# Kernel optimization log

Hardware: AMD Instinct MI355X
Metric: run time of the kernel (lower is better)

The kernel has to match this reference:

```python
import jax, jax.numpy as jnp
import numpy as np

N = 12288          # atoms
G = 12             # graphs in batch
R = 1536           # residues
K = 32             # max_num_neighbors
RADIUS = 5.0
MIN_DISTANCE = 5
EPS = 1e-10


def setup_inputs() -> dict:
    key = jax.random.key(0)
    k1, k2, k3 = jax.random.split(key, 3)
    # positions in a 50 A box -> protein-like density (~a few neighbors in r=5)
    node_position = jax.random.uniform(k1, (N, 3), dtype=jnp.float32) * 50.0
    node2graph = jnp.sort(jax.random.randint(k2, (N,), 0, G, dtype=jnp.int32))
    atom2residue = jnp.sort(jax.random.randint(k3, (N,), 0, R, dtype=jnp.int32))
    return {"node_position": node_position, "node2graph": node2graph,
            "atom2residue": atom2residue}


def _select_neighbors(node_position, node2graph):
    """For each node i, pick up to K nearest same-graph nodes within RADIUS.
    Returns idx [N,K] (neighbor indices) and in_radius [N,K] (validity)."""
    n = node_position.shape[0]
    sq = jnp.sum(node_position * node_position, axis=-1)            # [N]
    d2 = sq[:, None] + sq[None, :] - 2.0 * (node_position @ node_position.T)
    d2 = jnp.maximum(d2, 0.0)                                        # [N,N]
    ar = jnp.arange(n)
    valid = (node2graph[:, None] == node2graph[None, :]) \
            & (ar[:, None] != ar[None, :]) \
            & (d2 <= RADIUS * RADIUS)
    nd2 = jnp.where(valid, d2, jnp.inf)
    neg_d2, idx = jax.lax.top_k(-nd2, K)                             # nearest K
    in_radius = jnp.isfinite(neg_d2)
    return idx, in_radius


def reference(node_position, node2graph, atom2residue):
    n = node_position.shape[0]
    idx, in_radius = _select_neighbors(node_position, node2graph)
    node_out = jnp.repeat(jnp.arange(n, dtype=jnp.int32), K)         # center i
    node_in = idx.reshape(-1).astype(jnp.int32)                      # neighbor j
    valid = in_radius.reshape(-1)
    # residue-distance filter: drop |res_in - res_out| < min_distance
    res_diff = jnp.abs(atom2residue[node_in] - atom2residue[node_out])
    valid = valid & (res_diff >= MIN_DISTANCE)
    # drop near-coincident positions (||p_i - p_j|| < eps)
    diff = node_position[node_in] - node_position[node_out]
    d2_sel = jnp.sum(diff * diff, axis=-1)
    valid = valid & (d2_sel >= EPS * EPS)
    relation = jnp.zeros_like(node_in)
    edge_list = jnp.stack([node_in, node_out, relation], axis=-1)    # [N*K,3]
    edge_list = jnp.where(valid[:, None], edge_list, -1)             # pad invalid
    return edge_list, valid, jnp.int32(1)
```

## Files before the change

kernel.cpp:

```cpp
#include <hip/hip_runtime.h>

#define EDGE_K 32
#define CAP    128
#define NB     64

__global__ __launch_bounds__(256) void pack_kernel(
    const float* __restrict__ pos, const int* __restrict__ n2g,
    float4* __restrict__ pk, int* __restrict__ bounds, int n)
{
    int i = blockIdx.x * blockDim.x + threadIdx.x;
    if (i >= n) return;
    pk[i] = make_float4(pos[3*i+0], pos[3*i+1], pos[3*i+2], 0.0f);
    const int gi = n2g[i];
    if (i == 0) {
        for (int g = 0; g <= gi && g < NB; ++g) bounds[g] = 0;
    } else {
        const int gp = n2g[i-1];
        if (gp != gi) for (int g = gp + 1; g <= gi && g < NB; ++g) bounds[g] = i;
    }
    if (i == n - 1) {
        for (int g = gi + 1; g < NB; ++g) bounds[g] = n;
    }
}

__global__ __launch_bounds__(64) void spatial_edge_fast(
    const float4* __restrict__ pk,
    const int* __restrict__ n2g,
    const int* __restrict__ a2r,
    const int* __restrict__ bounds,
    int* __restrict__ out, int n)
{
    const int i    = blockIdx.x;
    const int lane = threadIdx.x;

    __shared__ int2 scand[CAP];
    __shared__ int2 sres[EDGE_K];

    const float4 pi = pk[i];
    const float xi = pi.x, yi = pi.y, zi = pi.z;
    const float si = xi*xi + yi*yi + zi*zi;
    const int g  = n2g[i];
    const int ri = a2r[i];

    int jstart, jend;
    if (g < NB - 1) {
        jstart = bounds[g];
        jend   = bounds[g + 1];
    } else {
        int lo = 0, hi = n;
        while (lo < hi) { int m = (lo + hi) >> 1; if (n2g[m] < g) lo = m + 1; else hi = m; }
        jstart = lo; hi = n;
        while (lo < hi) { int m = (lo + hi) >> 1; if (n2g[m] <= g) lo = m + 1; else hi = m; }
        jend = lo;
    }

    int count = 0;
    auto process = [&](float4 p, int j) {
        bool pass = false; float d2 = 0.0f;
        if (j < jend && j != i) {
            const float sj2 = p.x*p.x + p.y*p.y + p.z*p.z;
            const float dt  = xi*p.x + yi*p.y + zi*p.z;
            d2 = si + sj2 - 2.0f*dt;
            d2 = fmaxf(d2, 0.0f);
            pass = (d2 <= 25.0f);
        }
        const unsigned long long mask = __ballot(pass);
        if (pass) {
            const int idx = count +
                (int)__builtin_amdgcn_mbcnt_hi((unsigned)(mask >> 32),
                     __builtin_amdgcn_mbcnt_lo((unsigned)mask, 0u));
            if (idx < CAP) scand[idx] = make_int2(__float_as_int(d2), j);
        }
        count += __popcll(mask);
    };

    const int nch = (jend - jstart + 63) >> 6;
    const int jm  = jend - 1;
    for (int c = 0; c < nch; c += 4) {
        const int ja = jstart + (c << 6) + lane;
        const float4 p0 = pk[min(ja,       jm)];
        const float4 p1 = pk[min(ja +  64, jm)];
        const float4 p2 = pk[min(ja + 128, jm)];
        const float4 p3 = pk[min(ja + 192, jm)];
        process(p0, ja);
        if (c + 1 < nch) process(p1, ja + 64);
        if (c + 2 < nch) process(p2, ja + 128);
        if (c + 3 < nch) process(p3, ja + 192);
    }
    __syncthreads();

    int cnt = 0;
    if (count <= CAP) {
        const int m = count;
        for (int c = lane; c < m; c += 64) {
            const int2 e = scand[c];
            const float dc = __int_as_float(e.x);
            int rank = 0;
            for (int t = 0; t < m; ++t) {
                const int2 et = scand[t];
                const float dtv = __int_as_float(et.x);
                rank += (dtv < dc) || (dtv == dc && et.y < e.y);
            }
            if (rank < EDGE_K) sres[rank] = e;
        }
        cnt = (m < EDGE_K) ? m : EDGE_K;
    } else {
        if (lane == 0) {
            float bd[EDGE_K]; int bj[EDGE_K]; int c2 = 0;
            for (int j = jstart; j < jend; ++j) {
                if (j == i) continue;
                const float4 p = pk[j];
                const float sj2 = p.x*p.x + p.y*p.y + p.z*p.z;
                const float dt  = xi*p.x + yi*p.y + zi*p.z;
                float d2 = si + sj2 - 2.0f*dt;
                d2 = fmaxf(d2, 0.0f);
                if (d2 > 25.0f) continue;
                if (c2 == EDGE_K && d2 >= bd[EDGE_K-1]) continue;
                int p2 = (c2 < EDGE_K) ? c2 : (EDGE_K - 1);
                while (p2 > 0 && bd[p2-1] > d2) { bd[p2] = bd[p2-1]; bj[p2] = bj[p2-1]; --p2; }
                bd[p2] = d2; bj[p2] = j;
                if (c2 < EDGE_K) ++c2;
            }
            for (int k = 0; k < c2; ++k) sres[k] = make_int2(__float_as_int(bd[k]), bj[k]);
        }
        cnt = (count < EDGE_K) ? count : EDGE_K;
    }
    __syncthreads();

    const int NK = n * EDGE_K;
    int* valid_out = out + 3 * NK;
    if (lane < EDGE_K) {
        const int k = lane;
        int a = -1, b = -1, c = -1, v = 0;
        if (k < cnt) {
            const int j = sres[k].y;
            const int rj = a2r[j];
            const int rd = (rj > ri) ? (rj - ri) : (ri - rj);
            const float4 p = pk[j];
            const float dx = p.x - xi, dy = p.y - yi, dz = p.z - zi;
            const float d2s = dx*dx + dy*dy + dz*dz;
            if (rd >= 5 && d2s >= 1e-20f) { a = j; b = i; c = 0; v = 1; }
        }
        const int e = i * EDGE_K + k;
        out[3*e+0] = a;
        out[3*e+1] = b;
        out[3*e+2] = c;
        valid_out[e] = v;
    }
    if (i == 0 && lane == 0) out[4*NK] = 1;
}

__global__ __launch_bounds__(64) void spatial_edge_ref(
    const float* __restrict__ pos,
    const int* __restrict__ n2g,
    const int* __restrict__ a2r,
    int* __restrict__ out, int n)
{
    const int i = blockIdx.x;
    const int lane = threadIdx.x;
    __shared__ float sd2[CAP]; __shared__ int sj[CAP];
    __shared__ float rd2[EDGE_K]; __shared__ int rjj[EDGE_K];

    const float xi = pos[3*i+0], yi = pos[3*i+1], zi = pos[3*i+2];
    const float si = xi*xi + yi*yi + zi*zi;
    const int g = n2g[i]; const int ri = a2r[i];

    int lo = 0, hi = n;
    while (lo < hi) { int m = (lo + hi) >> 1; if (n2g[m] < g) lo = m + 1; else hi = m; }
    const int jstart = lo; hi = n;
    while (lo < hi) { int m = (lo + hi) >> 1; if (n2g[m] <= g) lo = m + 1; else hi = m; }
    const int jend = lo;

    int count = 0;
    for (int j0 = jstart; j0 < jend; j0 += 64) {
        const int j = j0 + lane;
        bool pass = false; float d2 = 0.0f;
        if (j < jend && j != i) {
            const float xj = pos[3*j+0], yj = pos[3*j+1], zj = pos[3*j+2];
            const float sj2 = xj*xj + yj*yj + zj*zj;
            const float dt  = xi*xj + yi*yj + zi*zj;
            d2 = fmaxf(si + sj2 - 2.0f*dt, 0.0f);
            pass = (d2 <= 25.0f);
        }
        const unsigned long long mask = __ballot(pass);
        if (pass) {
            const int idx = count + __popcll(mask & ((1ull << lane) - 1ull));
            if (idx < CAP) { sd2[idx] = d2; sj[idx] = j; }
        }
        count += __popcll(mask);
    }
    __syncthreads();

    int cnt;
    if (count <= CAP) {
        const int m = count;
        for (int c = lane; c < m; c += 64) {
            const float dc = sd2[c]; const int jc = sj[c];
            int rank = 0;
            for (int t = 0; t < m; ++t)
                rank += (sd2[t] < dc) || (sd2[t] == dc && sj[t] < jc);
            if (rank < EDGE_K) { rd2[rank] = dc; rjj[rank] = jc; }
        }
        cnt = (m < EDGE_K) ? m : EDGE_K;
    } else {
        if (lane == 0) {
            float bd[EDGE_K]; int bj[EDGE_K]; int c2 = 0;
            for (int j = jstart; j < jend; ++j) {
                if (j == i) continue;
                const float xj = pos[3*j+0], yj = pos[3*j+1], zj = pos[3*j+2];
                const float sj2 = xj*xj + yj*yj + zj*zj;
                const float dt  = xi*xj + yi*yj + zi*zj;
                float d2 = fmaxf(si + sj2 - 2.0f*dt, 0.0f);
                if (d2 > 25.0f) continue;
                if (c2 == EDGE_K && d2 >= bd[EDGE_K-1]) continue;
                int p = (c2 < EDGE_K) ? c2 : (EDGE_K - 1);
                while (p > 0 && bd[p-1] > d2) { bd[p] = bd[p-1]; bj[p] = bj[p-1]; --p; }
                bd[p] = d2; bj[p] = j;
                if (c2 < EDGE_K) ++c2;
            }
            for (int k = 0; k < c2; ++k) { rd2[k] = bd[k]; rjj[k] = bj[k]; }
        }
        cnt = (count < EDGE_K) ? count : EDGE_K;
    }
    __syncthreads();

    const int NK = n * EDGE_K;
    int* valid_out = out + 3 * NK;
    if (lane < EDGE_K) {
        const int k = lane;
        int a = -1, b = -1, c = -1, v = 0;
        if (k < cnt) {
            const int j = rjj[k];
            const int rj = a2r[j];
            const int rd = (rj > ri) ? (rj - ri) : (ri - rj);
            const float dx = pos[3*j+0] - xi, dy = pos[3*j+1] - yi, dz = pos[3*j+2] - zi;
            const float d2s = dx*dx + dy*dy + dz*dz;
            if (rd >= 5 && d2s >= 1e-20f) { a = j; b = i; c = 0; v = 1; }
        }
        const int e = i * EDGE_K + k;
        out[3*e+0] = a; out[3*e+1] = b; out[3*e+2] = c;
        valid_out[e] = v;
    }
    if (i == 0 && lane == 0) out[4*NK] = 1;
}

extern "C" void kernel_launch(void* const* d_in, const int* in_sizes, int n_in,
                              void* d_out, int out_size, void* d_ws, size_t ws_size,
                              hipStream_t stream) {
    const float* pos = (const float*)d_in[0];
    const int*   n2g = (const int*)d_in[1];
    const int*   a2r = (const int*)d_in[2];
    int* out = (int*)d_out;
    const int n = in_sizes[0] / 3;
    const size_t need = (size_t)n * sizeof(float4) + NB * sizeof(int);
    const bool packed = (ws_size >= need) && (((uintptr_t)d_ws & 15) == 0);
    if (packed) {
        float4* pk = (float4*)d_ws;
        int* bounds = (int*)(pk + n);
        hipLaunchKernelGGL(pack_kernel, dim3((n + 255) / 256), dim3(256), 0, stream,
                           pos, n2g, pk, bounds, n);
        hipLaunchKernelGGL(spatial_edge_fast, dim3(n), dim3(64), 0, stream,
                           (const float4*)pk, n2g, a2r, (const int*)bounds, out, n);
    } else {
        hipLaunchKernelGGL(spatial_edge_ref, dim3(n), dim3(64), 0, stream,
                           pos, n2g, a2r, out, n);
    }
}
```

Measured before the change: 29.86 us.

## Split per-atom candidate scan across four waves with per-wave candidate buffers

```diff
diff --git a/kernel.cpp b/kernel.cpp
--- a/kernel.cpp
+++ b/kernel.cpp
@@ -1,8 +1,16 @@
 #include <hip/hip_runtime.h>
 
 #define EDGE_K 32
+#define CAPW   64
 #define CAP    128
+#define WAVES  4
+#define BT     (64 * WAVES)
 #define NB     64
+
+__device__ __forceinline__ int prefix_count(unsigned long long mask) {
+    return (int)__builtin_amdgcn_mbcnt_hi((unsigned)(mask >> 32),
+                __builtin_amdgcn_mbcnt_lo((unsigned)mask, 0u));
+}
 
 __global__ __launch_bounds__(256) void pack_kernel(
     const float* __restrict__ pos, const int* __restrict__ n2g,
@@ -23,7 +31,7 @@
     }
 }
 
-__global__ __launch_bounds__(64) void spatial_edge_fast(
+__global__ __launch_bounds__(BT) void spatial_edge_fast(
     const float4* __restrict__ pk,
     const int* __restrict__ n2g,
     const int* __restrict__ a2r,
@@ -31,9 +39,12 @@
     int* __restrict__ out, int n)
 {
     const int i    = blockIdx.x;
-    const int lane = threadIdx.x;
-
-    __shared__ int2 scand[CAP];
+    const int tid  = threadIdx.x;
+    const int wave = tid >> 6;
+    const int lane = tid & 63;
+
+    __shared__ int2 scand[WAVES][CAPW];
+    __shared__ int  scnt[WAVES];
     __shared__ int2 sres[EDGE_K];
 
     const float4 pi = pk[i];
@@ -66,46 +77,59 @@
         }
         const unsigned long long mask = __ballot(pass);
         if (pass) {
-            const int idx = count +
-                (int)__builtin_amdgcn_mbcnt_hi((unsigned)(mask >> 32),
-                     __builtin_amdgcn_mbcnt_lo((unsigned)mask, 0u));
-            if (idx < CAP) scand[idx] = make_int2(__float_as_int(d2), j);
+            const int idx = count + prefix_count(mask);
+            if (idx < CAPW) scand[wave][idx] = make_int2(__float_as_int(d2), j);
         }
         count += __popcll(mask);
     };
 
-    const int nch = (jend - jstart + 63) >> 6;
-    const int jm  = jend - 1;
-    for (int c = 0; c < nch; c += 4) {
+    const int nch  = (jend - jstart + 63) >> 6;
+    const int nper = (nch + WAVES - 1) / WAVES;
+    const int cw0  = wave * nper;
+    const int cw1  = min(nch, cw0 + nper);
+    const int jm   = jend - 1;
+    for (int c = cw0; c < cw1; c += 4) {
         const int ja = jstart + (c << 6) + lane;
         const float4 p0 = pk[min(ja,       jm)];
         const float4 p1 = pk[min(ja +  64, jm)];
         const float4 p2 = pk[min(ja + 128, jm)];
         const float4 p3 = pk[min(ja + 192, jm)];
         process(p0, ja);
-        if (c + 1 < nch) process(p1, ja + 64);
-        if (c + 2 < nch) process(p2, ja + 128);
-        if (c + 3 < nch) process(p3, ja + 192);
-    }
-    __syncthreads();
-
-    int cnt = 0;
-    if (count <= CAP) {
-        const int m = count;
-        for (int c = lane; c < m; c += 64) {
-            const int2 e = scand[c];
+        if (c + 1 < cw1) process(p1, ja + 64);
+        if (c + 2 < cw1) process(p2, ja + 128);
+        if (c + 3 < cw1) process(p3, ja + 192);
+    }
+    if (lane == 0) scnt[wave] = count;
+    __syncthreads();
+
+    const int c0 = scnt[0], c1 = scnt[1], c2s = scnt[2], c3 = scnt[3];
+    const int total = c0 + c1 + c2s + c3;
+    const bool overflow = (c0 > CAPW) || (c1 > CAPW) || (c2s > CAPW) || (c3 > CAPW);
+
+    if (!overflow) {
+        const int cws[WAVES] = {c0, c1, c2s, c3};
+        for (int ft = tid; ft < total; ft += BT) {
+            int w2, cc;
+            if      (ft < c0)            { w2 = 0; cc = ft; }
+            else if (ft < c0 + c1)       { w2 = 1; cc = ft - c0; }
+            else if (ft < c0 + c1 + c2s) { w2 = 2; cc = ft - c0 - c1; }
+            else                         { w2 = 3; cc = ft - c0 - c1 - c2s; }
+            const int2 e = scand[w2][cc];
             const float dc = __int_as_float(e.x);
             int rank = 0;
-            for (int t = 0; t < m; ++t) {
-                const int2 et = scand[t];
-                const float dtv = __int_as_float(et.x);
-                rank += (dtv < dc) || (dtv == dc && et.y < e.y);
+#pragma unroll
+            for (int w3 = 0; w3 < WAVES; ++w3) {
+                const int cw = cws[w3];
+                for (int t2 = 0; t2 < cw; ++t2) {
+                    const int2 et = scand[w3][t2];
+                    const float dv = __int_as_float(et.x);
+                    rank += (dv < dc) || (dv == dc && et.y < e.y);
+                }
             }
             if (rank < EDGE_K) sres[rank] = e;
         }
-        cnt = (m < EDGE_K) ? m : EDGE_K;
-    } else {
-        if (lane == 0) {
+    } else {
+        if (tid == 0) {
             float bd[EDGE_K]; int bj[EDGE_K]; int c2 = 0;
             for (int j = jstart; j < jend; ++j) {
                 if (j == i) continue;
@@ -123,16 +147,16 @@
             }
             for (int k = 0; k < c2; ++k) sres[k] = make_int2(__float_as_int(bd[k]), bj[k]);
         }
-        cnt = (count < EDGE_K) ? count : EDGE_K;
-    }
-    __syncthreads();
-
+    }
+    __syncthreads();
+
+    const int cEff = (total < EDGE_K) ? total : EDGE_K;
     const int NK = n * EDGE_K;
     int* valid_out = out + 3 * NK;
-    if (lane < EDGE_K) {
-        const int k = lane;
+    if (tid < EDGE_K) {
+        const int k = tid;
         int a = -1, b = -1, c = -1, v = 0;
-        if (k < cnt) {
+        if (k < cEff) {
             const int j = sres[k].y;
             const int rj = a2r[j];
             const int rd = (rj > ri) ? (rj - ri) : (ri - rj);
@@ -147,7 +171,7 @@
         out[3*e+2] = c;
         valid_out[e] = v;
     }
-    if (i == 0 && lane == 0) out[4*NK] = 1;
+    if (i == 0 && tid == 0) out[4*NK] = 1;
 }
 
 __global__ __launch_bounds__(64) void spatial_edge_ref(
@@ -184,7 +208,7 @@
         }
         const unsigned long long mask = __ballot(pass);
         if (pass) {
-            const int idx = count + __popcll(mask & ((1ull << lane) - 1ull));
+            const int idx = count + prefix_count(mask);
             if (idx < CAP) { sd2[idx] = d2; sj[idx] = j; }
         }
         count += __popcll(mask);
@@ -259,7 +283,7 @@
         int* bounds = (int*)(pk + n);
         hipLaunchKernelGGL(pack_kernel, dim3((n + 255) / 256), dim3(256), 0, stream,
                            pos, n2g, pk, bounds, n);
-        hipLaunchKernelGGL(spatial_edge_fast, dim3(n), dim3(64), 0, stream,
+        hipLaunchKernelGGL(spatial_edge_fast, dim3(n), dim3(BT), 0, stream,
                            (const float4*)pk, n2g, a2r, (const int*)bounds, out, n);
     } else {
         hipLaunchKernelGGL(spatial_edge_ref, dim3(n), dim3(64), 0, stream,
```

After: 54.11 us. 81.2% more time.

## Software-pipeline candidate loads with depth-8 prefetch and coalesce edge output via LDS

Applied to the files above, without the earlier changes.

```diff
diff --git a/kernel.cpp b/kernel.cpp
--- a/kernel.cpp
+++ b/kernel.cpp
@@ -3,6 +3,12 @@
 #define EDGE_K 32
 #define CAP    128
 #define NB     64
+#define DEPTH  8
+
+__device__ __forceinline__ int prefix_count(unsigned long long mask) {
+    return (int)__builtin_amdgcn_mbcnt_hi((unsigned)(mask >> 32),
+                __builtin_amdgcn_mbcnt_lo((unsigned)mask, 0u));
+}
 
 __global__ __launch_bounds__(256) void pack_kernel(
     const float* __restrict__ pos, const int* __restrict__ n2g,
@@ -35,6 +41,7 @@
 
     __shared__ int2 scand[CAP];
     __shared__ int2 sres[EDGE_K];
+    __shared__ int2 ebuf2[EDGE_K * 3 / 2];
 
     const float4 pi = pk[i];
     const float xi = pi.x, yi = pi.y, zi = pi.z;
@@ -66,26 +73,34 @@
         }
         const unsigned long long mask = __ballot(pass);
         if (pass) {
-            const int idx = count +
-                (int)__builtin_amdgcn_mbcnt_hi((unsigned)(mask >> 32),
-                     __builtin_amdgcn_mbcnt_lo((unsigned)mask, 0u));
+            const int idx = count + prefix_count(mask);
             if (idx < CAP) scand[idx] = make_int2(__float_as_int(d2), j);
         }
         count += __popcll(mask);
     };
 
-    const int nch = (jend - jstart + 63) >> 6;
-    const int jm  = jend - 1;
-    for (int c = 0; c < nch; c += 4) {
+    const int nch  = (jend - jstart + 63) >> 6;
+    const int jm   = jend - 1;
+    const int base = jstart + lane;
+
+    float4 buf[DEPTH];
+#pragma unroll
+    for (int u = 0; u < DEPTH; ++u)
+        buf[u] = pk[min(base + (u << 6), jm)];
+
+    for (int c = 0; c < nch; c += DEPTH) {
+        float4 nxt[DEPTH];
+        const int nb = base + ((c + DEPTH) << 6);
+#pragma unroll
+        for (int u = 0; u < DEPTH; ++u)
+            nxt[u] = pk[min(nb + (u << 6), jm)];
         const int ja = jstart + (c << 6) + lane;
-        const float4 p0 = pk[min(ja,       jm)];
-        const float4 p1 = pk[min(ja +  64, jm)];
-        const float4 p2 = pk[min(ja + 128, jm)];
-        const float4 p3 = pk[min(ja + 192, jm)];
-        process(p0, ja);
-        if (c + 1 < nch) process(p1, ja + 64);
-        if (c + 2 < nch) process(p2, ja + 128);
-        if (c + 3 < nch) process(p3, ja + 192);
+#pragma unroll
+        for (int u = 0; u < DEPTH; ++u) {
+            if (c + u < nch) process(buf[u], ja + (u << 6));
+        }
+#pragma unroll
+        for (int u = 0; u < DEPTH; ++u) buf[u] = nxt[u];
     }
     __syncthreads();
 
@@ -129,6 +144,7 @@
 
     const int NK = n * EDGE_K;
     int* valid_out = out + 3 * NK;
+    int* eb = (int*)ebuf2;
     if (lane < EDGE_K) {
         const int k = lane;
         int a = -1, b = -1, c = -1, v = 0;
@@ -141,11 +157,15 @@
             const float d2s = dx*dx + dy*dy + dz*dz;
             if (rd >= 5 && d2s >= 1e-20f) { a = j; b = i; c = 0; v = 1; }
         }
-        const int e = i * EDGE_K + k;
-        out[3*e+0] = a;
-        out[3*e+1] = b;
-        out[3*e+2] = c;
-        valid_out[e] = v;
+        eb[3*k+0] = a;
+        eb[3*k+1] = b;
+        eb[3*k+2] = c;
+        valid_out[i * EDGE_K + k] = v;
+    }
+    __syncthreads();
+    if (lane < 48) {
+        int2* eo = (int2*)(out + 3 * (i * EDGE_K));
+        eo[lane] = ebuf2[lane];
     }
     if (i == 0 && lane == 0) out[4*NK] = 1;
 }
@@ -184,7 +204,7 @@
         }
         const unsigned long long mask = __ballot(pass);
         if (pass) {
-            const int idx = count + __popcll(mask & ((1ull << lane) - 1ull));
+            const int idx = count + prefix_count(mask);
             if (idx < CAP) { sd2[idx] = d2; sj[idx] = j; }
         }
         count += __popcll(mask);
```

Measured after the change: 29.23 us, median of 3. -2.1%, faster.
